# Performance work log

Hardware: AMD Instinct MI355X
Metric: run time of the kernel (lower is better)

## Reference

```python
import jax, jax.numpy as jnp
import numpy as np

D_MODEL = 1024
NHEAD = 16
HEAD_DIM = D_MODEL // NHEAD
D_FF = 4096
LN_EPS = 1e-5


def _layernorm(x, gamma, beta):
    mu = jnp.mean(x, axis=-1, keepdims=True)
    var = jnp.mean(jnp.square(x - mu), axis=-1, keepdims=True)
    return (x - mu) * jax.lax.rsqrt(var + LN_EPS) * gamma + beta


def setup_inputs() -> dict:
    key = jax.random.key(0)
    ks = jax.random.split(key, 16)
    s = 1.0 / np.sqrt(D_MODEL)
    sf = 1.0 / np.sqrt(D_FF)
    inp = {
        "src": jax.random.normal(ks[0], (2, 2048, D_MODEL), dtype=jnp.float32),
        # projection weights stored [in, out]
        "Wq": jax.random.uniform(ks[1], (D_MODEL, D_MODEL), minval=-s, maxval=s),
        "bq": jax.random.uniform(ks[2], (D_MODEL,), minval=-s, maxval=s),
        "Wk": jax.random.uniform(ks[3], (D_MODEL, D_MODEL), minval=-s, maxval=s),
        "bk": jax.random.uniform(ks[4], (D_MODEL,), minval=-s, maxval=s),
        "Wv": jax.random.uniform(ks[5], (D_MODEL, D_MODEL), minval=-s, maxval=s),
        "bv": jax.random.uniform(ks[6], (D_MODEL,), minval=-s, maxval=s),
        "Wo": jax.random.uniform(ks[7], (D_MODEL, D_MODEL), minval=-s, maxval=s),
        "bo": jax.random.uniform(ks[8], (D_MODEL,), minval=-s, maxval=s),
        "W1": jax.random.uniform(ks[9], (D_MODEL, D_FF), minval=-s, maxval=s),
        "b1": jax.random.uniform(ks[10], (D_FF,), minval=-s, maxval=s),
        "W2": jax.random.uniform(ks[11], (D_FF, D_MODEL), minval=-sf, maxval=sf),
        "b2": jax.random.uniform(ks[12], (D_MODEL,), minval=-sf, maxval=sf),
        "gamma1": jnp.ones((D_MODEL,), jnp.float32),
        "beta1": jnp.zeros((D_MODEL,), jnp.float32),
        "gamma2": jnp.ones((D_MODEL,), jnp.float32),
        "beta2": jnp.zeros((D_MODEL,), jnp.float32),
    }
    return inp


def reference(src, Wq, bq, Wk, bk, Wv, bv, Wo, bo, W1, b1, W2, b2,
              gamma1, beta1, gamma2, beta2):
    B, L, D = src.shape
    H, Hd = NHEAD, HEAD_DIM
    # QKV projections -> [B, H, L, Hd]
    def split_heads(x):
        return x.reshape(B, L, H, Hd).transpose(0, 2, 1, 3)
    Q = split_heads(src @ Wq + bq)
    K = split_heads(src @ Wk + bk)
    V = split_heads(src @ Wv + bv)
    # attention (dropout is eval-mode identity)
    scores = jnp.einsum("bhqd,bhkd->bhqk", Q, K) / np.sqrt(Hd)
    probs = jax.nn.softmax(scores, axis=-1)
    attn = jnp.einsum("bhqk,bhkd->bhqd", probs, V)
    attn = attn.transpose(0, 2, 1, 3).reshape(B, L, D)
    attn = attn @ Wo + bo
    x = _layernorm(src + attn, gamma1, beta1)
    ff = jax.nn.gelu(x @ W1 + b1, approximate=False) @ W2 + b2
    return _layernorm(x + ff, gamma2, beta2)
```

## Files before the change

### kernel.cpp

```cpp
#include <hip/hip_runtime.h>
#include <cstdint>
#include <cstddef>

using short8 = short __attribute__((ext_vector_type(8)));
using f32x4  = float __attribute__((ext_vector_type(4)));

__device__ __forceinline__ unsigned short f2bf(float f) {
  unsigned int u = __float_as_uint(f);
  u += 0x7fffu + ((u >> 16) & 1u);
  return (unsigned short)(u >> 16);
}
__device__ __forceinline__ float bf2f(unsigned short s) {
  return __uint_as_float(((unsigned int)s) << 16);
}
__device__ __forceinline__ unsigned int pack_bf16_rhu(float lo, float hi) {
  unsigned int a = __float_as_uint(lo) + 0x8000u;
  unsigned int b = __float_as_uint(hi) + 0x8000u;
  return __builtin_amdgcn_perm(b, a, 0x07060302u);
}
__device__ __forceinline__ void async16(const void* g, void* l) {
  __builtin_amdgcn_global_load_lds(
      (const __attribute__((address_space(1))) unsigned int*)g,
      (__attribute__((address_space(3))) unsigned int*)l, 16, 0, 0);
}

#define D_MODEL 1024
#define NHEAD   16
#define HEADD   64
#define SEQL    2048
#define NTOK    4096
#define QSCALE  0.18033688011112042f

struct TransTab {
  const float* src[6];
  unsigned short* dst[6];
  int R[6], C[6], start[6], shift[6];
  const float* cvt_in;
  unsigned short* cvt_out;
};

__global__ __launch_bounds__(256) void prep_all(TransTab tt) {
  __shared__ float tile[32][33];
  int id = blockIdx.x;
  if (id < 4096) {
    int i = id * 256 + threadIdx.x;
    float4 v = ((const float4*)tt.cvt_in)[i];
    union { unsigned long long u; unsigned int ui[2]; } pk;
    pk.ui[0] = pack_bf16_rhu(v.x, v.y);
    pk.ui[1] = pack_bf16_rhu(v.z, v.w);
    ((unsigned long long*)tt.cvt_out)[i] = pk.u;
    return;
  }
  id -= 4096;
  int m = 0;
#pragma unroll
  for (int i = 1; i < 6; ++i) if (id >= tt.start[i]) m = i;
  const int local = id - tt.start[m];
  const int R = tt.R[m], C = tt.C[m];
  const int bc = (local & ((1 << tt.shift[m]) - 1)) * 32;
  const int br = (local >> tt.shift[m]) * 32;
  const float* in = tt.src[m];
  unsigned short* out = tt.dst[m];
  const int tx = threadIdx.x & 31, ty = threadIdx.x >> 5;
#pragma unroll
  for (int i = 0; i < 32; i += 8)
    tile[ty + i][tx] = in[(size_t)(br + ty + i) * C + bc + tx];
  __syncthreads();
#pragma unroll
  for (int i = 0; i < 32; i += 8)
    out[(size_t)(bc + ty + i) * R + br + tx] = f2bf(tile[tx][ty + i]);
}

template <int MODE>
__global__ __launch_bounds__(256, 4)
void gemm_bt(const unsigned short* __restrict__ A, const unsigned short* __restrict__ B,
             int M, int N, int K, int Kstride,
             const float* __restrict__ bias0, const float* __restrict__ bias1,
             const float* __restrict__ bias2,
             float* __restrict__ outF, unsigned short* __restrict__ outB,
             unsigned short* __restrict__ outQ, unsigned short* __restrict__ outK,
             unsigned short* __restrict__ outVT) {
  __shared__ __align__(16) short sA[128 * 64];
  __shared__ __align__(16) short sB[128 * 64];
  const int tid = threadIdx.x, wave = tid >> 6, lane = tid & 63;
  const int quad = lane >> 4, l16 = lane & 15;
  const int bm = blockIdx.y * 128, bn = blockIdx.x * 128;
  const int koff = blockIdx.z * K;
  const int wr = (wave >> 1) * 64, wc = (wave & 1) * 64;
  const f32x4 zero4 = {0.f, 0.f, 0.f, 0.f};
  f32x4 acc[4][4];
#pragma unroll
  for (int i = 0; i < 4; ++i)
#pragma unroll
    for (int j = 0; j < 4; ++j) acc[i][j] = zero4;

  for (int kt = 0; kt < K; kt += 64) {
    __syncthreads();
#pragma unroll
    for (int j = 0; j < 4; ++j) {
      int c = (wave * 4 + j) * 64 + lane;
      int row = c >> 3, cp = c & 7;
      int gk = koff + kt + ((cp ^ (row & 7)) * 8);
      async16(A + (size_t)(bm + row) * Kstride + gk, &sA[(wave * 4 + j) * 512]);
      async16(B + (size_t)(bn + row) * Kstride + gk, &sB[(wave * 4 + j) * 512]);
    }
    __syncthreads();
#pragma unroll
    for (int kk = 0; kk < 2; ++kk) {
      short8 af[4], bfr[4];
#pragma unroll
      for (int i = 0; i < 4; ++i) {
        int ra = wr + i * 16 + l16;
        af[i] = *(const short8*)&sA[ra * 64 + (((kk * 4 + quad) ^ (ra & 7)) * 8)];
        int rb = wc + i * 16 + l16;
        bfr[i] = *(const short8*)&sB[rb * 64 + (((kk * 4 + quad) ^ (rb & 7)) * 8)];
      }
#pragma unroll
      for (int mi = 0; mi < 4; ++mi)
#pragma unroll
        for (int ni = 0; ni < 4; ++ni)
          acc[mi][ni] = __builtin_amdgcn_mfma_f32_16x16x32_bf16(af[mi], bfr[ni], acc[mi][ni], 0, 0, 0);
    }
  }

#pragma unroll
  for (int mi = 0; mi < 4; ++mi)
#pragma unroll
    for (int ni = 0; ni < 4; ++ni) {
      const int col = bn + wc + ni * 16 + l16;
      const int row0 = bm + wr + mi * 16 + quad * 4;
      if constexpr (MODE == 0) {
        const int b_ = row0 >> 11, l_ = row0 & 2047;
        if (col < 1024) {
          const int hh = col >> 6, dd = col & 63;
          const size_t o = (((size_t)(b_ * NHEAD + hh)) * SEQL + l_) * HEADD + dd;
#pragma unroll
          for (int r = 0; r < 4; ++r)
            outQ[o + (size_t)r * HEADD] = f2bf((acc[mi][ni][r] + bias0[col]) * QSCALE);
        } else if (col < 2048) {
          const int n2 = col - 1024, hh = n2 >> 6, dd = n2 & 63;
          const size_t o = (((size_t)(b_ * NHEAD + hh)) * SEQL + l_) * HEADD + dd;
#pragma unroll
          for (int r = 0; r < 4; ++r)
            outK[o + (size_t)r * HEADD] = f2bf(acc[mi][ni][r] + bias1[n2]);
        } else {
          const int n2 = col - 2048, hh = n2 >> 6, dd = n2 & 63;
          union { unsigned long long u; unsigned short us[4]; } pk;
#pragma unroll
          for (int r = 0; r < 4; ++r) pk.us[r] = f2bf(acc[mi][ni][r] + bias2[n2]);
          *(unsigned long long*)&outVT[(((size_t)(b_ * NHEAD + hh)) * HEADD + dd) * SEQL + l_] = pk.u;
        }
      } else if constexpr (MODE == 1) {
        float* o = outF + (size_t)blockIdx.z * M * N + (size_t)row0 * N + col;
#pragma unroll
        for (int r = 0; r < 4; ++r) o[(size_t)r * N] = acc[mi][ni][r];
      } else {
#pragma unroll
        for (int r = 0; r < 4; ++r) {
          float x = acc[mi][ni][r] + bias0[col];
          float x2 = x * x;
          float z = x * fmaf(0.102944f, x2, 2.302208f);
          float t = __builtin_amdgcn_exp2f(z);
          float gl = x - x * __builtin_amdgcn_rcpf(t + 1.0f);
          outB[(size_t)(row0 + r) * N + col] = f2bf(gl);
        }
      }
    }
}

__global__ __launch_bounds__(512, 4)
void flash_attn(const unsigned short* __restrict__ Qb, const unsigned short* __restrict__ Kb,
                const unsigned short* __restrict__ VTb, unsigned short* __restrict__ attnA) {
  __shared__ __align__(16) short sK[128 * 64];
  __shared__ __align__(16) short sV[64 * 128];
  __shared__ __align__(16) short sP[8 * 32 * 72];
  __shared__ float lred[4][32];
  const int tid = threadIdx.x, wave = tid >> 6, lane = tid & 63;
  const int quad = lane >> 4, l16 = lane & 15;
  const int wq = wave >> 1;
  const int wk = wave & 1;
  const int bh = blockIdx.y;
  const int q0 = blockIdx.x * 128;
  const size_t baseQK = (size_t)bh * SEQL * HEADD;
  const size_t baseV  = (size_t)bh * HEADD * SEQL;
  const int pbase = wave * (32 * 72);

#pragma unroll
  for (int j = 0; j < 2; ++j) {
    int c = (wave * 2 + j) * 64 + lane;
    int row = c >> 3, cp = c & 7;
    int gk = (cp ^ (row & 7)) * 8;
    async16(Qb + baseQK + (size_t)(q0 + row) * HEADD + gk, &sK[(wave * 2 + j) * 512]);
  }
  __syncthreads();
  short8 qf[2][2];
#pragma unroll
  for (int mi = 0; mi < 2; ++mi)
#pragma unroll
    for (int kk = 0; kk < 2; ++kk) {
      int m = wq * 32 + mi * 16 + l16;
      qf[mi][kk] = *(const short8*)&sK[m * 64 + (((kk * 4 + quad) ^ (m & 7)) * 8)];
    }

  const f32x4 zero4 = {0.f, 0.f, 0.f, 0.f};
  f32x4 o_acc[2][4];
  float lsum[2] = {0.f, 0.f};
#pragma unroll
  for (int mi = 0; mi < 2; ++mi)
#pragma unroll
    for (int ni = 0; ni < 4; ++ni) o_acc[mi][ni] = zero4;

  for (int t0 = 0; t0 < SEQL; t0 += 128) {
    __syncthreads();
#pragma unroll
    for (int j = 0; j < 2; ++j) {
      int c = (wave * 2 + j) * 64 + lane;
      { int row = c >> 3, cp = c & 7;
        int gk = (cp ^ (row & 7)) * 8;
        async16(Kb + baseQK + (size_t)(t0 + row) * HEADD + gk, &sK[(wave * 2 + j) * 512]); }
      { int d = c >> 4, cp = c & 15;
        int gl = (cp ^ (d & 15)) * 8;
        async16(VTb + baseV + (size_t)d * SEQL + t0 + gl, &sV[(wave * 2 + j) * 512]); }
    }
    __syncthreads();

    f32x4 st[4][2];
#pragma unroll
    for (int kt = 0; kt < 4; ++kt)
#pragma unroll
      for (int mi = 0; mi < 2; ++mi) st[kt][mi] = zero4;
#pragma unroll
    for (int kt = 0; kt < 4; ++kt) {
      int krow = wk * 64 + kt * 16 + l16;
      short8 a0 = *(const short8*)&sK[krow * 64 + ((quad ^ (krow & 7)) * 8)];
      short8 a1 = *(const short8*)&sK[krow * 64 + (((4 + quad) ^ (krow & 7)) * 8)];
#pragma unroll
      for (int mi = 0; mi < 2; ++mi) {
        st[kt][mi] = __builtin_amdgcn_mfma_f32_16x16x32_bf16(a0, qf[mi][0], st[kt][mi], 0, 0, 0);
        st[kt][mi] = __builtin_amdgcn_mfma_f32_16x16x32_bf16(a1, qf[mi][1], st[kt][mi], 0, 0, 0);
      }
    }
#pragma unroll
    for (int kt = 0; kt < 4; ++kt)
#pragma unroll
      for (int mi = 0; mi < 2; ++mi) {
        float e0 = __builtin_amdgcn_exp2f(st[kt][mi][0]);
        float e1 = __builtin_amdgcn_exp2f(st[kt][mi][1]);
        float e2 = __builtin_amdgcn_exp2f(st[kt][mi][2]);
        float e3 = __builtin_amdgcn_exp2f(st[kt][mi][3]);
        lsum[mi] += (e0 + e1) + (e2 + e3);
        union { unsigned long long u; unsigned int ui[2]; } pk;
        pk.ui[0] = pack_bf16_rhu(e0, e1);
        pk.ui[1] = pack_bf16_rhu(e2, e3);
        *(unsigned long long*)&sP[pbase + (mi * 16 + l16) * 72 + kt * 16 + quad * 4] = pk.u;
      }
#pragma unroll
    for (int c = 0; c < 2; ++c) {
      short8 vf[4];
#pragma unroll
      for (int ni = 0; ni < 4; ++ni) {
        int vrow = ni * 16 + l16;
        vf[ni] = *(const short8*)&sV[vrow * 128 + (((wk * 8 + c * 4 + quad) ^ (vrow & 15)) * 8)];
      }
#pragma unroll
      for (int mi = 0; mi < 2; ++mi) {
        short8 pf = *(const short8*)&sP[pbase + (mi * 16 + l16) * 72 + c * 32 + quad * 8];
#pragma unroll
        for (int ni = 0; ni < 4; ++ni)
          o_acc[mi][ni] = __builtin_amdgcn_mfma_f32_16x16x32_bf16(pf, vf[ni], o_acc[mi][ni], 0, 0, 0);
      }
    }
  }

#pragma unroll
  for (int mi = 0; mi < 2; ++mi) {
    lsum[mi] += __shfl_xor(lsum[mi], 16, 64);
    lsum[mi] += __shfl_xor(lsum[mi], 32, 64);
  }
  __syncthreads();
  float* op = (float*)sP;
  if (wk == 1) {
    float* dst = op + wq * (64 * 36);
#pragma unroll
    for (int mi = 0; mi < 2; ++mi)
#pragma unroll
      for (int ni = 0; ni < 4; ++ni)
        *(f32x4*)&dst[(ni * 16 + l16) * 36 + mi * 16 + quad * 4] = o_acc[mi][ni];
    if (quad == 0) {
      lred[wq][l16] = lsum[0];
      lred[wq][16 + l16] = lsum[1];
    }
  }
  __syncthreads();
  if (wk == 0) {
    const float* srcp = op + wq * (64 * 36);
    const int b_ = bh >> 4, hh = bh & 15;
#pragma unroll
    for (int mi = 0; mi < 2; ++mi) {
      float ltot = lsum[mi] + lred[wq][mi * 16 + l16];
#pragma unroll
      for (int ni = 0; ni < 4; ++ni) {
        f32x4 other = *(const f32x4*)&srcp[(ni * 16 + l16) * 36 + mi * 16 + quad * 4];
        o_acc[mi][ni] += other;
      }
#pragma unroll
      for (int r = 0; r < 4; ++r) {
        float inv = 1.0f / __shfl(ltot, quad * 4 + r, 64);
        int qrow = q0 + wq * 32 + mi * 16 + quad * 4 + r;
        size_t orow = ((size_t)(b_ * SEQL + qrow)) * D_MODEL + hh * HEADD;
#pragma unroll
        for (int ni = 0; ni < 4; ++ni)
          attnA[orow + ni * 16 + l16] = f2bf(o_acc[mi][ni][r] * inv);
      }
    }
  }
}

__device__ __forceinline__ void ln_core(float x0, float x1, float x2, float x3,
                                        const float* gamma, const float* beta,
                                        int tid, float& y0, float& y1, float& y2, float& y3) {
  float s = x0 + x1 + x2 + x3;
  float q = x0 * x0 + x1 * x1 + x2 * x2 + x3 * x3;
#pragma unroll
  for (int m = 1; m < 64; m <<= 1) {
    s += __shfl_xor(s, m, 64);
    q += __shfl_xor(q, m, 64);
  }
  __shared__ float red[8];
  const int wv = tid >> 6, ln = tid & 63;
  if (ln == 0) { red[wv] = s; red[4 + wv] = q; }
  __syncthreads();
  float S = red[0] + red[1] + red[2] + red[3];
  float Q2 = red[4] + red[5] + red[6] + red[7];
  float mu = S * (1.0f / 1024.0f);
  float var = Q2 * (1.0f / 1024.0f) - mu * mu;
  float rstd = rsqrtf(var + 1e-5f);
  float4 g = ((const float4*)gamma)[tid];
  float4 b = ((const float4*)beta)[tid];
  y0 = (x0 - mu) * rstd * g.x + b.x;
  y1 = (x1 - mu) * rstd * g.y + b.y;
  y2 = (x2 - mu) * rstd * g.z + b.z;
  y3 = (x3 - mu) * rstd * g.w + b.w;
}

__global__ __launch_bounds__(256)
void ln_combine1(const float* __restrict__ p, const float* __restrict__ src,
                 const float* __restrict__ bias, const float* __restrict__ gamma,
                 const float* __restrict__ beta, unsigned short* __restrict__ outB) {
  const int t = blockIdx.x, tid = threadIdx.x;
  const size_t MN = (size_t)NTOK * 1024, base = (size_t)t * 1024;
  float4 a = ((const float4*)(p + base))[tid];
  float4 b4 = ((const float4*)(p + MN + base))[tid];
  a.x += b4.x; a.y += b4.y; a.z += b4.z; a.w += b4.w;
  float4 s4 = ((const float4*)(src + base))[tid];
  float4 bi = ((const float4*)bias)[tid];
  float y0, y1, y2, y3;
  ln_core(a.x + s4.x + bi.x, a.y + s4.y + bi.y,
          a.z + s4.z + bi.z, a.w + s4.w + bi.w,
          gamma, beta, tid, y0, y1, y2, y3);
  union { unsigned long long u; unsigned int ui[2]; } pk;
  pk.ui[0] = (unsigned)f2bf(y0) | ((unsigned)f2bf(y1) << 16);
  pk.ui[1] = (unsigned)f2bf(y2) | ((unsigned)f2bf(y3) << 16);
  ((unsigned long long*)(outB + base))[tid] = pk.u;
}

__global__ __launch_bounds__(256)
void ln_combine2(const float* __restrict__ p, const unsigned short* __restrict__ resB,
                 const float* __restrict__ bias, const float* __restrict__ gamma,
                 const float* __restrict__ beta, float* __restrict__ outF) {
  const int t = blockIdx.x, tid = threadIdx.x;
  const size_t MN = (size_t)NTOK * 1024, base = (size_t)t * 1024;
  float4 a = ((const float4*)(p + base))[tid];
  float4 b4 = ((const float4*)(p + MN + base))[tid];
  a.x += b4.x; a.y += b4.y; a.z += b4.z; a.w += b4.w;
  union { unsigned long long u; unsigned short us[4]; } r;
  r.u = ((const unsigned long long*)(resB + base))[tid];
  float4 bi = ((const float4*)bias)[tid];
  float y0, y1, y2, y3;
  ln_core(a.x + bf2f(r.us[0]) + bi.x, a.y + bf2f(r.us[1]) + bi.y,
          a.z + bf2f(r.us[2]) + bi.z, a.w + bf2f(r.us[3]) + bi.w,
          gamma, beta, tid, y0, y1, y2, y3);
  float4 o = {y0, y1, y2, y3};
  ((float4*)(outF + base))[tid] = o;
}

extern "C" void kernel_launch(void* const* d_in, const int* in_sizes, int n_in,
                              void* d_out, int out_size, void* d_ws, size_t ws_size,
                              hipStream_t stream) {
  const float* src    = (const float*)d_in[0];
  const float* Wq     = (const float*)d_in[1];
  const float* bq     = (const float*)d_in[2];
  const float* Wk     = (const float*)d_in[3];
  const float* bk     = (const float*)d_in[4];
  const float* Wv     = (const float*)d_in[5];
  const float* bv     = (const float*)d_in[6];
  const float* Wo     = (const float*)d_in[7];
  const float* bo     = (const float*)d_in[8];
  const float* W1     = (const float*)d_in[9];
  const float* b1     = (const float*)d_in[10];
  const float* W2     = (const float*)d_in[11];
  const float* b2     = (const float*)d_in[12];
  const float* gamma1 = (const float*)d_in[13];
  const float* beta1  = (const float*)d_in[14];
  const float* gamma2 = (const float*)d_in[15];
  const float* beta2  = (const float*)d_in[16];
  float* out = (float*)d_out;
  (void)in_sizes; (void)n_in; (void)out_size; (void)ws_size;

  char* p = (char*)d_ws;
  auto carve = [&](size_t n) { char* r = p; p += (n + 255) & ~(size_t)255; return r; };
  unsigned short* srcB  = (unsigned short*)carve((size_t)NTOK * 1024 * 2);
  unsigned short* WqkvT = (unsigned short*)carve((size_t)3072 * 1024 * 2);
  unsigned short* WoT   = (unsigned short*)carve((size_t)1024 * 1024 * 2);
  unsigned short* W1T   = (unsigned short*)carve((size_t)4096 * 1024 * 2);
  unsigned short* W2T   = (unsigned short*)carve((size_t)1024 * 4096 * 2);
  unsigned short* Qb    = (unsigned short*)carve((size_t)NTOK * 1024 * 2);
  unsigned short* Kb    = (unsigned short*)carve((size_t)NTOK * 1024 * 2);
  unsigned short* VTb   = (unsigned short*)carve((size_t)NTOK * 1024 * 2);
  carve((size_t)NTOK * 1024 * 2);
  unsigned short* xln   = (unsigned short*)carve((size_t)NTOK * 1024 * 2);
  unsigned short* hmid  = (unsigned short*)carve((size_t)NTOK * 4096 * 2);
  unsigned short* attnA = srcB;
  float* partial = (float*)Qb;

  TransTab tt;
  tt.src[0] = Wq; tt.src[1] = Wk; tt.src[2] = Wv; tt.src[3] = Wo; tt.src[4] = W1; tt.src[5] = W2;
  tt.dst[0] = WqkvT; tt.dst[1] = WqkvT + 1024 * 1024; tt.dst[2] = WqkvT + 2 * 1024 * 1024;
  tt.dst[3] = WoT; tt.dst[4] = W1T; tt.dst[5] = W2T;
  for (int i = 0; i < 4; ++i) { tt.R[i] = 1024; tt.C[i] = 1024; tt.shift[i] = 5; }
  tt.R[4] = 1024; tt.C[4] = 4096; tt.shift[4] = 7;
  tt.R[5] = 4096; tt.C[5] = 1024; tt.shift[5] = 5;
  tt.start[0] = 0; tt.start[1] = 1024; tt.start[2] = 2048; tt.start[3] = 3072;
  tt.start[4] = 4096; tt.start[5] = 8192;
  tt.cvt_in = src; tt.cvt_out = srcB;
  prep_all<<<16384, 256, 0, stream>>>(tt);

  gemm_bt<0><<<dim3(24, 32, 1), 256, 0, stream>>>(srcB, WqkvT, NTOK, 3072, 1024, 1024,
                                                  bq, bk, bv, nullptr, nullptr, Qb, Kb, VTb);
  flash_attn<<<dim3(16, 32), 512, 0, stream>>>(Qb, Kb, VTb, attnA);
  gemm_bt<1><<<dim3(8, 32, 2), 256, 0, stream>>>(attnA, WoT, NTOK, 1024, 512, 1024,
                                                 nullptr, nullptr, nullptr, partial,
                                                 nullptr, nullptr, nullptr, nullptr);
  ln_combine1<<<NTOK, 256, 0, stream>>>(partial, src, bo, gamma1, beta1, xln);
  gemm_bt<2><<<dim3(32, 32, 1), 256, 0, stream>>>(xln, W1T, NTOK, 4096, 1024, 1024,
                                                  b1, nullptr, nullptr, nullptr, hmid,
                                                  nullptr, nullptr, nullptr);
  gemm_bt<1><<<dim3(8, 32, 2), 256, 0, stream>>>(hmid, W2T, NTOK, 1024, 2048, 4096,
                                                 nullptr, nullptr, nullptr, partial,
                                                 nullptr, nullptr, nullptr, nullptr);
  ln_combine2<<<NTOK, 256, 0, stream>>>(partial, xln, b2, gamma2, beta2, out);
}
```

Measured before the change: 338.1 us.

## Split attention across two KV halves with separate merge kernel

Flash attention now splits the key sequence into two halves via a third grid dimension, writing unnormalized partial outputs and row sums to a workspace. A new merge kernel sums the partials, normalizes and writes the bf16 attention output. The P staging buffer is shrunk by interleaving exp/pack with the PV MFMAs per 32-key chunk, allowing higher occupancy. The aim is to fill more CUs; it adds extra fp32 traffic and a kernel launch.

```diff
diff --git a/kernel.cpp b/kernel.cpp
--- a/kernel.cpp
+++ b/kernel.cpp
@@ -168,22 +168,24 @@
     }
 }
 
-__global__ __launch_bounds__(512, 4)
+__global__ __launch_bounds__(512, 6)
 void flash_attn(const unsigned short* __restrict__ Qb, const unsigned short* __restrict__ Kb,
-                const unsigned short* __restrict__ VTb, unsigned short* __restrict__ attnA) {
-  __shared__ __align__(16) short sK[128 * 64];
-  __shared__ __align__(16) short sV[64 * 128];
-  __shared__ __align__(16) short sP[8 * 32 * 72];
-  __shared__ float lred[4][32];
+                const unsigned short* __restrict__ VTb,
+                float* __restrict__ pO, float* __restrict__ pL) {
+  __shared__ __align__(16) short smem[26624];
+  short* sK = smem;
+  short* sV = smem + 8192;
+  short* sP = smem + 16384;
   const int tid = threadIdx.x, wave = tid >> 6, lane = tid & 63;
   const int quad = lane >> 4, l16 = lane & 15;
   const int wq = wave >> 1;
   const int wk = wave & 1;
   const int bh = blockIdx.y;
   const int q0 = blockIdx.x * 128;
+  const int t0base = blockIdx.z * 1024;
   const size_t baseQK = (size_t)bh * SEQL * HEADD;
   const size_t baseV  = (size_t)bh * HEADD * SEQL;
-  const int pbase = wave * (32 * 72);
+  const int pbase = wave * (32 * 40);
 
 #pragma unroll
   for (int j = 0; j < 2; ++j) {
@@ -210,7 +212,7 @@
 #pragma unroll
     for (int ni = 0; ni < 4; ++ni) o_acc[mi][ni] = zero4;
 
-  for (int t0 = 0; t0 < SEQL; t0 += 128) {
+  for (int t0 = t0base; t0 < t0base + 1024; t0 += 128) {
     __syncthreads();
 #pragma unroll
     for (int j = 0; j < 2; ++j) {
@@ -241,21 +243,22 @@
       }
     }
 #pragma unroll
-    for (int kt = 0; kt < 4; ++kt)
-#pragma unroll
-      for (int mi = 0; mi < 2; ++mi) {
-        float e0 = __builtin_amdgcn_exp2f(st[kt][mi][0]);
-        float e1 = __builtin_amdgcn_exp2f(st[kt][mi][1]);
-        float e2 = __builtin_amdgcn_exp2f(st[kt][mi][2]);
-        float e3 = __builtin_amdgcn_exp2f(st[kt][mi][3]);
-        lsum[mi] += (e0 + e1) + (e2 + e3);
-        union { unsigned long long u; unsigned int ui[2]; } pk;
-        pk.ui[0] = pack_bf16_rhu(e0, e1);
-        pk.ui[1] = pack_bf16_rhu(e2, e3);
-        *(unsigned long long*)&sP[pbase + (mi * 16 + l16) * 72 + kt * 16 + quad * 4] = pk.u;
-      }
-#pragma unroll
     for (int c = 0; c < 2; ++c) {
+#pragma unroll
+      for (int kt2 = 0; kt2 < 2; ++kt2)
+#pragma unroll
+        for (int mi = 0; mi < 2; ++mi) {
+          f32x4 sv = st[c * 2 + kt2][mi];
+          float e0 = __builtin_amdgcn_exp2f(sv[0]);
+          float e1 = __builtin_amdgcn_exp2f(sv[1]);
+          float e2 = __builtin_amdgcn_exp2f(sv[2]);
+          float e3 = __builtin_amdgcn_exp2f(sv[3]);
+          lsum[mi] += (e0 + e1) + (e2 + e3);
+          union { unsigned long long u; unsigned int ui[2]; } pk;
+          pk.ui[0] = pack_bf16_rhu(e0, e1);
+          pk.ui[1] = pack_bf16_rhu(e2, e3);
+          *(unsigned long long*)&sP[pbase + (mi * 16 + l16) * 40 + kt2 * 16 + quad * 4] = pk.u;
+        }
       short8 vf[4];
 #pragma unroll
       for (int ni = 0; ni < 4; ++ni) {
@@ -264,7 +267,7 @@
       }
 #pragma unroll
       for (int mi = 0; mi < 2; ++mi) {
-        short8 pf = *(const short8*)&sP[pbase + (mi * 16 + l16) * 72 + c * 32 + quad * 8];
+        short8 pf = *(const short8*)&sP[pbase + (mi * 16 + l16) * 40 + quad * 8];
 #pragma unroll
         for (int ni = 0; ni < 4; ++ni)
           o_acc[mi][ni] = __builtin_amdgcn_mfma_f32_16x16x32_bf16(pf, vf[ni], o_acc[mi][ni], 0, 0, 0);
@@ -278,7 +281,8 @@
     lsum[mi] += __shfl_xor(lsum[mi], 32, 64);
   }
   __syncthreads();
-  float* op = (float*)sP;
+  float* op = (float*)smem;
+  float* lred = (float*)&smem[24576];
   if (wk == 1) {
     float* dst = op + wq * (64 * 36);
 #pragma unroll
@@ -287,32 +291,53 @@
       for (int ni = 0; ni < 4; ++ni)
         *(f32x4*)&dst[(ni * 16 + l16) * 36 + mi * 16 + quad * 4] = o_acc[mi][ni];
     if (quad == 0) {
-      lred[wq][l16] = lsum[0];
-      lred[wq][16 + l16] = lsum[1];
+      lred[wq * 32 + l16] = lsum[0];
+      lred[wq * 32 + 16 + l16] = lsum[1];
     }
   }
   __syncthreads();
   if (wk == 0) {
     const float* srcp = op + wq * (64 * 36);
-    const int b_ = bh >> 4, hh = bh & 15;
+    const int bl = blockIdx.z * 512 + bh * 16 + blockIdx.x;
+    float* po = pO + (size_t)bl * 8192;
 #pragma unroll
     for (int mi = 0; mi < 2; ++mi) {
-      float ltot = lsum[mi] + lred[wq][mi * 16 + l16];
+      float ltot = lsum[mi] + lred[wq * 32 + mi * 16 + l16];
+      if (quad == 0) pL[(size_t)bl * 128 + wq * 32 + mi * 16 + l16] = ltot;
 #pragma unroll
       for (int ni = 0; ni < 4; ++ni) {
         f32x4 other = *(const f32x4*)&srcp[(ni * 16 + l16) * 36 + mi * 16 + quad * 4];
-        o_acc[mi][ni] += other;
-      }
-#pragma unroll
-      for (int r = 0; r < 4; ++r) {
-        float inv = 1.0f / __shfl(ltot, quad * 4 + r, 64);
-        int qrow = q0 + wq * 32 + mi * 16 + quad * 4 + r;
-        size_t orow = ((size_t)(b_ * SEQL + qrow)) * D_MODEL + hh * HEADD;
-#pragma unroll
-        for (int ni = 0; ni < 4; ++ni)
-          attnA[orow + ni * 16 + l16] = f2bf(o_acc[mi][ni][r] * inv);
-      }
-    }
+        f32x4 tot = o_acc[mi][ni] + other;
+#pragma unroll
+        for (int r = 0; r < 4; ++r)
+          po[(size_t)(wq * 32 + mi * 16 + quad * 4 + r) * 64 + ni * 16 + l16] = tot[r];
+      }
+    }
+  }
+}
+
+__global__ __launch_bounds__(256)
+void attn_merge(const float* __restrict__ pO, const float* __restrict__ pL,
+                unsigned short* __restrict__ attnA) {
+  const int bh = blockIdx.x >> 4, qb = blockIdx.x & 15;
+  const int b_ = bh >> 4, h = bh & 15;
+  const int tid = threadIdx.x;
+  const int qloc = tid >> 1, dbase = (tid & 1) * 32;
+  const int bl0 = bh * 16 + qb, bl1 = 512 + bh * 16 + qb;
+  const float l = pL[(size_t)bl0 * 128 + qloc] + pL[(size_t)bl1 * 128 + qloc];
+  const float inv = 1.0f / l;
+  const float* p0 = pO + (size_t)bl0 * 8192 + qloc * 64 + dbase;
+  const float* p1 = pO + (size_t)bl1 * 8192 + qloc * 64 + dbase;
+  const int token = b_ * SEQL + qb * 128 + qloc;
+  unsigned short* o = attnA + (size_t)token * D_MODEL + h * HEADD + dbase;
+#pragma unroll
+  for (int v = 0; v < 8; ++v) {
+    f32x4 a = *(const f32x4*)(p0 + v * 4);
+    f32x4 b = *(const f32x4*)(p1 + v * 4);
+    union { unsigned long long u; unsigned int ui[2]; } pk;
+    pk.ui[0] = pack_bf16_rhu((a[0] + b[0]) * inv, (a[1] + b[1]) * inv);
+    pk.ui[1] = pack_bf16_rhu((a[2] + b[2]) * inv, (a[3] + b[3]) * inv);
+    *(unsigned long long*)(o + v * 4) = pk.u;
   }
 }
 
@@ -420,6 +445,8 @@
   carve((size_t)NTOK * 1024 * 2);
   unsigned short* xln   = (unsigned short*)carve((size_t)NTOK * 1024 * 2);
   unsigned short* hmid  = (unsigned short*)carve((size_t)NTOK * 4096 * 2);
+  float*          pO    = (float*)carve((size_t)1024 * 8192 * 4);
+  float*          pL    = (float*)carve((size_t)1024 * 128 * 4);
   unsigned short* attnA = srcB;
   float* partial = (float*)Qb;
 
@@ -437,7 +464,8 @@
 
   gemm_bt<0><<<dim3(24, 32, 1), 256, 0, stream>>>(srcB, WqkvT, NTOK, 3072, 1024, 1024,
                                                   bq, bk, bv, nullptr, nullptr, Qb, Kb, VTb);
-  flash_attn<<<dim3(16, 32), 512, 0, stream>>>(Qb, Kb, VTb, attnA);
+  flash_attn<<<dim3(16, 32, 2), 512, 0, stream>>>(Qb, Kb, VTb, pO, pL);
+  attn_merge<<<512, 256, 0, stream>>>(pO, pL, attnA);
   gemm_bt<1><<<dim3(8, 32, 2), 256, 0, stream>>>(attnA, WoT, NTOK, 1024, 512, 1024,
                                                  nullptr, nullptr, nullptr, partial,
                                                  nullptr, nullptr, nullptr, nullptr);
```

New measurement: 483.9 us. 1.43x slower.
